# Performance work log

Hardware: AMD Instinct MI355X
Metric: run time of the kernel (lower is better)

The kernel has to match this reference:

```python
import jax, jax.numpy as jnp
import numpy as np

# Constraint of the (buggy) original module: batch N == num_heads H == embed_size E, head_dim = 1,
# and value_len == key_len == query_len == L.
E = 64   # embed_size == num_heads == batch
H = 64
N = 64
L = 256
LN_EPS = 1e-5


def setup_inputs() -> dict:
    key = jax.random.key(0)
    ks = jax.random.split(key, 4)
    return {
        "values": jax.random.normal(ks[0], (N, L, E), dtype=jnp.float32),
        "keys": jax.random.normal(ks[1], (N, L, E), dtype=jnp.float32),
        "query": jax.random.normal(ks[2], (N, L, E), dtype=jnp.float32),
        # fc_out params (torch nn.Linear: y = x @ W.T + b)
        "W_out": jax.random.normal(ks[3], (E, E), dtype=jnp.float32) / np.float32(np.sqrt(E)),
        "b_out": jnp.zeros((E,), dtype=jnp.float32),
        # LayerNorm params
        "ln_w": jnp.ones((E,), dtype=jnp.float32),
        "ln_b": jnp.zeros((E,), dtype=jnp.float32),
    }


def reference(values, keys, query, W_out, b_out, ln_w, ln_b):
    Nb, Lq, Emb = query.shape
    Hh = H
    hd = Emb // Hh  # == 1

    def split_heads(x):
        # [N, L, E] -> [N, L, H, hd] -> permute(2,0,1,3) -> [H, N, L, hd]
        return x.reshape(Nb, -1, Hh, hd).transpose(2, 0, 1, 3)

    v = split_heads(values)   # [H, N, Lv, hd]
    k = split_heads(keys)     # [H, N, Lk, hd]
    q = split_heads(query)    # [H, N, Lq, hd]

    # torch.einsum('qnhd,knhd->qnk') on [H,N,L,hd] tensors: contract over (seq, head_dim)
    energy = jnp.einsum('anld,bnld->anb', q, k)            # [H, N, H]
    attn = jax.nn.softmax(energy / jnp.sqrt(jnp.float32(hd)), axis=-1)

    # torch.einsum('qnk,nkhd->qnhd') with values [H,N,Lv,hd]; requires N == H
    out = jnp.einsum('qnk,nkld->qnld', attn, v)            # [H, N, Lv, hd]

    # permute(1,2,0,3) -> [N, Lv, H, hd] -> view(N, Lq, E)
    out = out.transpose(1, 2, 0, 3).reshape(Nb, Lq, Emb)
    out = out @ W_out.T + b_out                            # fc_out, [N, Lq, E]

    # residual against the PERMUTED query [H,N,L,1] broadcasts to [H, N, Lq, E]
    x = out + q

    mu = jnp.mean(x, axis=-1, keepdims=True)
    var = jnp.var(x, axis=-1, keepdims=True)
    return (x - mu) / jnp.sqrt(var + LN_EPS) * ln_w + ln_b
```

## Files before the change

### kernel.cpp

```cpp
#include <hip/hip_runtime.h>
#include <stdint.h>

#define L_SEQ 256
#define E_DIM 64
#define N_B   64
#define LN_EPS 1e-5f

typedef float f4 __attribute__((ext_vector_type(4)));

__global__ __launch_bounds__(256) void fused_row_kernel(
    const float* __restrict__ gq,
    const float* __restrict__ gk,
    const float* __restrict__ gv,
    const float* __restrict__ gw,
    const float* __restrict__ gbo,
    const float* __restrict__ glnw,
    const float* __restrict__ glnb,
    float*       __restrict__ ws)
{
    __shared__ float lds[32768];
    float* Qs    = lds;
    float* Ks    = lds + 16384;
    float* VnS   = lds;
    float* attnS = lds + 16384;
    float* WtS   = lds + 20480;
    float* PS    = lds + 24576;

    const int t = threadIdx.x;
    const int n = blockIdx.x;
    const float* qb = gq + (size_t)n * (L_SEQ * E_DIM);
    const float* kb = gk + (size_t)n * (L_SEQ * E_DIM);

    #pragma unroll
    for (int i = 0; i < 16; ++i) {
        reinterpret_cast<f4*>(Qs)[t + 256 * i] =
            reinterpret_cast<const f4*>(qb)[t + 256 * i];
        reinterpret_cast<f4*>(Ks)[t + 256 * i] =
            reinterpret_cast<const f4*>(kb)[t + 256 * i];
    }
    __syncthreads();

    const int tx = t & 15, ty = t >> 4;
    const int b0 = tx * 4, a0 = ty * 4;

    float acc[4][4] = {};
    #pragma unroll 8
    for (int l = 0; l < L_SEQ; ++l) {
        f4 qa = *reinterpret_cast<const f4*>(&Qs[l * E_DIM + a0]);
        f4 kv = *reinterpret_cast<const f4*>(&Ks[l * E_DIM + b0]);
        #pragma unroll
        for (int ia = 0; ia < 4; ++ia)
            #pragma unroll
            for (int ib = 0; ib < 4; ++ib)
                acc[ia][ib] = fmaf(qa[ia], kv[ib], acc[ia][ib]);
    }

    #pragma unroll
    for (int ia = 0; ia < 4; ++ia) {
        float m = fmaxf(fmaxf(acc[ia][0], acc[ia][1]),
                        fmaxf(acc[ia][2], acc[ia][3]));
        #pragma unroll
        for (int s = 1; s <= 8; s <<= 1) m = fmaxf(m, __shfl_xor(m, s));
        float e0v = __expf(acc[ia][0] - m);
        float e1v = __expf(acc[ia][1] - m);
        float e2v = __expf(acc[ia][2] - m);
        float e3v = __expf(acc[ia][3] - m);
        float ssum = (e0v + e1v) + (e2v + e3v);
        #pragma unroll
        for (int s = 1; s <= 8; s <<= 1) ssum += __shfl_xor(ssum, s);
        float inv = 1.0f / ssum;
        acc[ia][0] = e0v * inv; acc[ia][1] = e1v * inv;
        acc[ia][2] = e2v * inv; acc[ia][3] = e3v * inv;
    }

    __syncthreads();

    #pragma unroll
    for (int ia = 0; ia < 4; ++ia) {
        f4 v4 = {acc[ia][0], acc[ia][1], acc[ia][2], acc[ia][3]};
        *reinterpret_cast<f4*>(&attnS[(a0 + ia) * 64 + b0]) = v4;
    }

    #pragma unroll
    for (int i = 0; i < 16; ++i) {
        int idx = t + 256 * i;
        WtS[(idx & 63) * 64 + (idx >> 6)] = gw[idx];
    }

    #pragma unroll
    for (int k = 0; k < 64; ++k)
        VnS[k * 256 + t] = gv[((size_t)k * 256 + (size_t)t) * 64 + n];

    __syncthreads();

    const int k0 = ty * 4, e0 = tx * 4;
    float pacc[4][4] = {};
    #pragma unroll 8
    for (int q = 0; q < 64; ++q) {
        f4 av = *reinterpret_cast<const f4*>(&attnS[q * 64 + k0]);
        f4 wv = *reinterpret_cast<const f4*>(&WtS[q * 64 + e0]);
        #pragma unroll
        for (int ik = 0; ik < 4; ++ik)
            #pragma unroll
            for (int ie = 0; ie < 4; ++ie)
                pacc[ik][ie] = fmaf(av[ik], wv[ie], pacc[ik][ie]);
    }
    #pragma unroll
    for (int ik = 0; ik < 4; ++ik) {
        f4 v4 = {pacc[ik][0], pacc[ik][1], pacc[ik][2], pacc[ik][3]};
        *reinterpret_cast<f4*>(&PS[(k0 + ik) * 64 + e0]) = v4;
    }

    f4 be = *reinterpret_cast<const f4*>(&gbo[e0]);
    f4 lw = *reinterpret_cast<const f4*>(&glnw[e0]);
    f4 lb = *reinterpret_cast<const f4*>(&glnb[e0]);

    __syncthreads();

    const int l0 = ty * 16;
    float fcv[16][4] = {};
    #pragma unroll 4
    for (int k = 0; k < 64; ++k) {
        f4 p4 = *reinterpret_cast<const f4*>(&PS[k * 64 + e0]);
        f4 vv[4];
        #pragma unroll
        for (int g = 0; g < 4; ++g)
            vv[g] = *reinterpret_cast<const f4*>(&VnS[k * 256 + l0 + 4 * g]);
        #pragma unroll
        for (int g = 0; g < 4; ++g)
            #pragma unroll
            for (int j = 0; j < 4; ++j)
                #pragma unroll
                for (int ie = 0; ie < 4; ++ie)
                    fcv[g * 4 + j][ie] = fmaf(vv[g][j], p4[ie], fcv[g * 4 + j][ie]);
    }

    float* wbase = ws + (size_t)n * 16384 + (size_t)l0 * 64 + e0;
    #pragma unroll
    for (int il = 0; il < 16; ++il) {
        float v0 = fcv[il][0] + be[0];
        float v1 = fcv[il][1] + be[1];
        float v2 = fcv[il][2] + be[2];
        float v3 = fcv[il][3] + be[3];
        float s1 = (v0 + v1) + (v2 + v3);
        float s2 = (v0 * v0 + v1 * v1) + (v2 * v2 + v3 * v3);
        #pragma unroll
        for (int s = 1; s <= 8; s <<= 1) {
            s1 += __shfl_xor(s1, s);
            s2 += __shfl_xor(s2, s);
        }
        float mu  = s1 * (1.0f / 64.0f);
        float var = s2 * (1.0f / 64.0f) - mu * mu;
        float rs  = rsqrtf(var + LN_EPS);
        f4 o;
        o[0] = (v0 - mu) * rs * lw[0] + lb[0];
        o[1] = (v1 - mu) * rs * lw[1] + lb[1];
        o[2] = (v2 - mu) * rs * lw[2] + lb[2];
        o[3] = (v3 - mu) * rs * lw[3] + lb[3];
        *reinterpret_cast<f4*>(wbase + (size_t)il * 64) = o;
    }
}

__global__ __launch_bounds__(256) void bcast_kernel(
    const float* __restrict__ ws,
    float*       __restrict__ gout)
{
    const int t  = threadIdx.x;
    const int b  = blockIdx.x;
    const int n  = b >> 4;
    const int lc = b & 15;
    const int r  = t >> 4;
    const int c  = t & 15;

    const size_t row = (size_t)n * 16384 + (size_t)(lc * 16 + r) * 64
                     + (size_t)c * 4;
    f4 v = *reinterpret_cast<const f4*>(ws + row);

    float* op = gout + row;
    #pragma unroll
    for (int h = 0; h < 64; ++h) {
        __builtin_nontemporal_store(v, reinterpret_cast<f4*>(op));
        op += (size_t)N_B * L_SEQ * E_DIM;
    }
}

extern "C" void kernel_launch(void* const* d_in, const int* in_sizes, int n_in,
                              void* d_out, int out_size, void* d_ws, size_t ws_size,
                              hipStream_t stream)
{
    const float* gv  = (const float*)d_in[0];
    const float* gk  = (const float*)d_in[1];
    const float* gq  = (const float*)d_in[2];
    const float* gw  = (const float*)d_in[3];
    const float* gbo = (const float*)d_in[4];
    const float* glw = (const float*)d_in[5];
    const float* glb = (const float*)d_in[6];
    float* wsRow = (float*)d_ws;
    float* out   = (float*)d_out;

    hipLaunchKernelGGL(fused_row_kernel, dim3(64), dim3(256), 0, stream,
                       gq, gk, gv, gw, gbo, glw, glb, wsRow);
    hipLaunchKernelGGL(bcast_kernel, dim3(1024), dim3(256), 0, stream,
                       wsRow, out);
}
```

Measured before the change: 329.7 us.

## Move V-gather, fc and LayerNorm into the wide broadcast kernel

Splits the work so that the 64-block kernel only computes attention and P = attn·Wᵀ, using 512 threads per block, and writes P to the workspace. The second kernel, with 1024 blocks, gathers its slice of V, computes fc, applies LayerNorm and broadcasts to all heads directly. This spreads the strided V gather and the fc math over many more blocks and removes the intermediate row round trip. In exchange, each broadcast block re-reads P, and the W LDS layout is padded to reduce bank conflicts.

Result: faster. 311.4 us (-5.5%).

```diff
diff --git a/kernel.cpp b/kernel.cpp
--- a/kernel.cpp
+++ b/kernel.cpp
@@ -7,24 +7,19 @@
 #define LN_EPS 1e-5f
 
 typedef float f4 __attribute__((ext_vector_type(4)));
-
-__global__ __launch_bounds__(256) void fused_row_kernel(
+typedef float f2 __attribute__((ext_vector_type(2)));
+
+__global__ __launch_bounds__(512) void attn_p_kernel(
     const float* __restrict__ gq,
     const float* __restrict__ gk,
-    const float* __restrict__ gv,
     const float* __restrict__ gw,
-    const float* __restrict__ gbo,
-    const float* __restrict__ glnw,
-    const float* __restrict__ glnb,
-    float*       __restrict__ ws)
+    float*       __restrict__ wsP)
 {
     __shared__ float lds[32768];
     float* Qs    = lds;
     float* Ks    = lds + 16384;
-    float* VnS   = lds;
-    float* attnS = lds + 16384;
-    float* WtS   = lds + 20480;
-    float* PS    = lds + 24576;
+    float* attnS = lds;
+    float* WtS   = lds + 4096;
 
     const int t = threadIdx.x;
     const int n = blockIdx.x;
@@ -32,31 +27,31 @@
     const float* kb = gk + (size_t)n * (L_SEQ * E_DIM);
 
     #pragma unroll
-    for (int i = 0; i < 16; ++i) {
-        reinterpret_cast<f4*>(Qs)[t + 256 * i] =
-            reinterpret_cast<const f4*>(qb)[t + 256 * i];
-        reinterpret_cast<f4*>(Ks)[t + 256 * i] =
-            reinterpret_cast<const f4*>(kb)[t + 256 * i];
+    for (int i = 0; i < 8; ++i) {
+        reinterpret_cast<f4*>(Qs)[t + 512 * i] =
+            reinterpret_cast<const f4*>(qb)[t + 512 * i];
+        reinterpret_cast<f4*>(Ks)[t + 512 * i] =
+            reinterpret_cast<const f4*>(kb)[t + 512 * i];
     }
     __syncthreads();
 
     const int tx = t & 15, ty = t >> 4;
-    const int b0 = tx * 4, a0 = ty * 4;
-
-    float acc[4][4] = {};
+    const int b0 = tx * 4, a0 = ty * 2;
+
+    float acc[2][4] = {};
     #pragma unroll 8
     for (int l = 0; l < L_SEQ; ++l) {
-        f4 qa = *reinterpret_cast<const f4*>(&Qs[l * E_DIM + a0]);
+        f2 qa = *reinterpret_cast<const f2*>(&Qs[l * E_DIM + a0]);
         f4 kv = *reinterpret_cast<const f4*>(&Ks[l * E_DIM + b0]);
         #pragma unroll
-        for (int ia = 0; ia < 4; ++ia)
+        for (int ia = 0; ia < 2; ++ia)
             #pragma unroll
             for (int ib = 0; ib < 4; ++ib)
                 acc[ia][ib] = fmaf(qa[ia], kv[ib], acc[ia][ib]);
     }
 
     #pragma unroll
-    for (int ia = 0; ia < 4; ++ia) {
+    for (int ia = 0; ia < 2; ++ia) {
         float m = fmaxf(fmaxf(acc[ia][0], acc[ia][1]),
                         fmaxf(acc[ia][2], acc[ia][3]));
         #pragma unroll
@@ -76,111 +71,114 @@
     __syncthreads();
 
     #pragma unroll
-    for (int ia = 0; ia < 4; ++ia) {
+    for (int ia = 0; ia < 2; ++ia) {
         f4 v4 = {acc[ia][0], acc[ia][1], acc[ia][2], acc[ia][3]};
         *reinterpret_cast<f4*>(&attnS[(a0 + ia) * 64 + b0]) = v4;
     }
 
     #pragma unroll
-    for (int i = 0; i < 16; ++i) {
-        int idx = t + 256 * i;
-        WtS[(idx & 63) * 64 + (idx >> 6)] = gw[idx];
-    }
-
-    #pragma unroll
-    for (int k = 0; k < 64; ++k)
-        VnS[k * 256 + t] = gv[((size_t)k * 256 + (size_t)t) * 64 + n];
-
-    __syncthreads();
-
-    const int k0 = ty * 4, e0 = tx * 4;
-    float pacc[4][4] = {};
+    for (int i = 0; i < 8; ++i) {
+        int idx = t + 512 * i;
+        WtS[(idx & 63) * 68 + (idx >> 6)] = gw[idx];
+    }
+    __syncthreads();
+
+    const int k0 = ty * 2, e0 = tx * 4;
+    float pacc[2][4] = {};
     #pragma unroll 8
     for (int q = 0; q < 64; ++q) {
-        f4 av = *reinterpret_cast<const f4*>(&attnS[q * 64 + k0]);
-        f4 wv = *reinterpret_cast<const f4*>(&WtS[q * 64 + e0]);
-        #pragma unroll
-        for (int ik = 0; ik < 4; ++ik)
+        f2 av = *reinterpret_cast<const f2*>(&attnS[q * 64 + k0]);
+        f4 wv = *reinterpret_cast<const f4*>(&WtS[q * 68 + e0]);
+        #pragma unroll
+        for (int ik = 0; ik < 2; ++ik)
             #pragma unroll
             for (int ie = 0; ie < 4; ++ie)
                 pacc[ik][ie] = fmaf(av[ik], wv[ie], pacc[ik][ie]);
     }
-    #pragma unroll
-    for (int ik = 0; ik < 4; ++ik) {
+    float* pb = wsP + (size_t)n * 4096 + e0;
+    #pragma unroll
+    for (int ik = 0; ik < 2; ++ik) {
         f4 v4 = {pacc[ik][0], pacc[ik][1], pacc[ik][2], pacc[ik][3]};
-        *reinterpret_cast<f4*>(&PS[(k0 + ik) * 64 + e0]) = v4;
+        *reinterpret_cast<f4*>(pb + (size_t)(k0 + ik) * 64) = v4;
+    }
+}
+
+__global__ __launch_bounds__(256) void fc_ln_bcast_kernel(
+    const float* __restrict__ gv,
+    const float* __restrict__ gbo,
+    const float* __restrict__ glnw,
+    const float* __restrict__ glnb,
+    const float* __restrict__ wsP,
+    float*       __restrict__ gout)
+{
+    __shared__ float PS[64 * 64];
+    __shared__ float VnS[64 * 16];
+
+    const int t  = threadIdx.x;
+    const int b  = blockIdx.x;
+    const int n  = b >> 4;
+    const int l0 = (b & 15) * 16;
+
+    const f4* psrc = reinterpret_cast<const f4*>(wsP + (size_t)n * 4096);
+    #pragma unroll
+    for (int i = 0; i < 4; ++i)
+        reinterpret_cast<f4*>(PS)[t + 256 * i] = psrc[t + 256 * i];
+
+    #pragma unroll
+    for (int i = 0; i < 4; ++i) {
+        int idx = t + 256 * i;
+        int lp = idx & 15, k = idx >> 4;
+        VnS[k * 16 + lp] =
+            gv[(size_t)k * (L_SEQ * E_DIM) + (size_t)(l0 + lp) * E_DIM + n];
+    }
+    __syncthreads();
+
+    const int tx = t & 15, ty = t >> 4;
+    const int e0 = tx * 4;
+
+    float fc0 = 0.f, fc1 = 0.f, fc2 = 0.f, fc3 = 0.f;
+    #pragma unroll 8
+    for (int k = 0; k < 64; ++k) {
+        float v = VnS[k * 16 + ty];
+        f4 p4 = *reinterpret_cast<const f4*>(&PS[k * 64 + e0]);
+        fc0 = fmaf(v, p4[0], fc0);
+        fc1 = fmaf(v, p4[1], fc1);
+        fc2 = fmaf(v, p4[2], fc2);
+        fc3 = fmaf(v, p4[3], fc3);
     }
 
     f4 be = *reinterpret_cast<const f4*>(&gbo[e0]);
     f4 lw = *reinterpret_cast<const f4*>(&glnw[e0]);
     f4 lb = *reinterpret_cast<const f4*>(&glnb[e0]);
 
-    __syncthreads();
-
-    const int l0 = ty * 16;
-    float fcv[16][4] = {};
-    #pragma unroll 4
-    for (int k = 0; k < 64; ++k) {
-        f4 p4 = *reinterpret_cast<const f4*>(&PS[k * 64 + e0]);
-        f4 vv[4];
-        #pragma unroll
-        for (int g = 0; g < 4; ++g)
-            vv[g] = *reinterpret_cast<const f4*>(&VnS[k * 256 + l0 + 4 * g]);
-        #pragma unroll
-        for (int g = 0; g < 4; ++g)
-            #pragma unroll
-            for (int j = 0; j < 4; ++j)
-                #pragma unroll
-                for (int ie = 0; ie < 4; ++ie)
-                    fcv[g * 4 + j][ie] = fmaf(vv[g][j], p4[ie], fcv[g * 4 + j][ie]);
-    }
-
-    float* wbase = ws + (size_t)n * 16384 + (size_t)l0 * 64 + e0;
-    #pragma unroll
-    for (int il = 0; il < 16; ++il) {
-        float v0 = fcv[il][0] + be[0];
-        float v1 = fcv[il][1] + be[1];
-        float v2 = fcv[il][2] + be[2];
-        float v3 = fcv[il][3] + be[3];
-        float s1 = (v0 + v1) + (v2 + v3);
-        float s2 = (v0 * v0 + v1 * v1) + (v2 * v2 + v3 * v3);
-        #pragma unroll
-        for (int s = 1; s <= 8; s <<= 1) {
-            s1 += __shfl_xor(s1, s);
-            s2 += __shfl_xor(s2, s);
-        }
-        float mu  = s1 * (1.0f / 64.0f);
-        float var = s2 * (1.0f / 64.0f) - mu * mu;
-        float rs  = rsqrtf(var + LN_EPS);
-        f4 o;
-        o[0] = (v0 - mu) * rs * lw[0] + lb[0];
-        o[1] = (v1 - mu) * rs * lw[1] + lb[1];
-        o[2] = (v2 - mu) * rs * lw[2] + lb[2];
-        o[3] = (v3 - mu) * rs * lw[3] + lb[3];
-        *reinterpret_cast<f4*>(wbase + (size_t)il * 64) = o;
-    }
-}
-
-__global__ __launch_bounds__(256) void bcast_kernel(
-    const float* __restrict__ ws,
-    float*       __restrict__ gout)
-{
-    const int t  = threadIdx.x;
-    const int b  = blockIdx.x;
-    const int n  = b >> 4;
-    const int lc = b & 15;
-    const int r  = t >> 4;
-    const int c  = t & 15;
-
-    const size_t row = (size_t)n * 16384 + (size_t)(lc * 16 + r) * 64
-                     + (size_t)c * 4;
-    f4 v = *reinterpret_cast<const f4*>(ws + row);
-
-    float* op = gout + row;
-    #pragma unroll
+    float v0 = fc0 + be[0];
+    float v1 = fc1 + be[1];
+    float v2 = fc2 + be[2];
+    float v3 = fc3 + be[3];
+
+    float s1 = (v0 + v1) + (v2 + v3);
+    float s2 = (v0 * v0 + v1 * v1) + (v2 * v2 + v3 * v3);
+    #pragma unroll
+    for (int s = 1; s <= 8; s <<= 1) {
+        s1 += __shfl_xor(s1, s);
+        s2 += __shfl_xor(s2, s);
+    }
+    float mu  = s1 * (1.0f / 64.0f);
+    float var = s2 * (1.0f / 64.0f) - mu * mu;
+    float rs  = rsqrtf(var + LN_EPS);
+    f4 o;
+    o[0] = (v0 - mu) * rs * lw[0] + lb[0];
+    o[1] = (v1 - mu) * rs * lw[1] + lb[1];
+    o[2] = (v2 - mu) * rs * lw[2] + lb[2];
+    o[3] = (v3 - mu) * rs * lw[3] + lb[3];
+
+    float* op = gout + (size_t)n * (L_SEQ * E_DIM)
+                     + (size_t)(l0 + ty) * E_DIM + e0;
+    const size_t hstride = (size_t)N_B * L_SEQ * E_DIM;
+    #pragma unroll 8
     for (int h = 0; h < 64; ++h) {
-        __builtin_nontemporal_store(v, reinterpret_cast<f4*>(op));
-        op += (size_t)N_B * L_SEQ * E_DIM;
+        __builtin_nontemporal_store(o, reinterpret_cast<f4*>(op));
+        op += hstride;
     }
 }
 
@@ -195,11 +193,11 @@
     const float* gbo = (const float*)d_in[4];
     const float* glw = (const float*)d_in[5];
     const float* glb = (const float*)d_in[6];
-    float* wsRow = (float*)d_ws;
-    float* out   = (float*)d_out;
-
-    hipLaunchKernelGGL(fused_row_kernel, dim3(64), dim3(256), 0, stream,
-                       gq, gk, gv, gw, gbo, glw, glb, wsRow);
-    hipLaunchKernelGGL(bcast_kernel, dim3(1024), dim3(256), 0, stream,
-                       wsRow, out);
+    float* wsP = (float*)d_ws;
+    float* out = (float*)d_out;
+
+    hipLaunchKernelGGL(attn_p_kernel, dim3(64), dim3(512), 0, stream,
+                       gq, gk, gw, wsP);
+    hipLaunchKernelGGL(fc_ln_bcast_kernel, dim3(1024), dim3(256), 0, stream,
+                       gv, gbo, glw, glb, wsP, out);
 }
```
